# Performance work log

Hardware: AMD Instinct MI355X
Metric: run time of the kernel (lower is better)

## Reference

```python
import math
import jax, jax.numpy as jnp
import numpy as np

SIZE = 512
N_HEADS = 8
HEAD = SIZE // N_HEADS
SCALE = 1.0 / math.sqrt(HEAD)


def setup_inputs() -> dict:
    key = jax.random.key(0)
    ks = jax.random.split(key, 10)
    B, Sq, Skv = 4, 2048, 2048
    std = 1.0 / math.sqrt(SIZE)
    inp = {
        "query": jax.random.normal(ks[0], (B, Sq, SIZE), jnp.float32),
        "key_value": jax.random.normal(ks[1], (B, Skv, SIZE), jnp.float32),
        "Wq": jax.random.normal(ks[2], (SIZE, SIZE), jnp.float32) * std,
        "bq": jax.random.normal(ks[3], (SIZE,), jnp.float32) * std,
        "Wk": jax.random.normal(ks[4], (SIZE, SIZE), jnp.float32) * std,
        "bk": jax.random.normal(ks[5], (SIZE,), jnp.float32) * std,
        "Wv": jax.random.normal(ks[6], (SIZE, SIZE), jnp.float32) * std,
        "bv": jax.random.normal(ks[7], (SIZE,), jnp.float32) * std,
        "Wo": jax.random.normal(ks[8], (SIZE, SIZE), jnp.float32) * std,
        "bo": jax.random.normal(ks[9], (SIZE,), jnp.float32) * std,
    }
    return inp


def reference(query, key_value, Wq, bq, Wk, bk, Wv, bv, Wo, bo):
    B, Sq, D = query.shape
    Skv = key_value.shape[1]
    H, hd = N_HEADS, HEAD

    # Linear projections (torch nn.Linear: x @ W.T + b)
    q = query @ Wq.T + bq            # [B, Sq, D]
    k = key_value @ Wk.T + bk        # [B, Skv, D]
    v = key_value @ Wv.T + bv        # [B, Skv, D]

    # split heads: [B, S, H, hd]
    qh = q.reshape(B, Sq, H, hd)
    kh = k.reshape(B, Skv, H, hd)
    vh = v.reshape(B, Skv, H, hd)

    # attention scores and softmax over keys
    scores = jnp.einsum("bqhd,bkhd->bhqk", qh, kh) * SCALE  # [B, H, Sq, Skv]
    A = jax.nn.softmax(scores, axis=-1)
    o = jnp.einsum("bhqk,bkhd->bqhd", A, vh)                 # [B, Sq, H, hd]

    # residual with q heads (clean_path=False), merge heads
    out = (qh + o).reshape(B, Sq, D)

    # output residual + ReLU FFN stage
    out = out + jax.nn.relu(out @ Wo.T + bo)
    return out
```

## Files before the change

kernel.cpp:

```cpp
#include <hip/hip_runtime.h>
#include <hip/hip_bf16.h>

typedef __hip_bfloat16 bf16;
typedef __attribute__((ext_vector_type(4))) float f32x4;
typedef __attribute__((ext_vector_type(16))) float f32x16;
typedef __attribute__((ext_vector_type(8))) __bf16 bf16x8;

#define DEVI static __device__ __forceinline__

DEVI void gload_lds16(const void* g, void* l) {
  __builtin_amdgcn_global_load_lds(
      (const __attribute__((address_space(1))) void*)g,
      (__attribute__((address_space(3))) void*)l, 16, 0, 0);
}

DEVI unsigned pkbf(float a, float b) {
  union { __hip_bfloat162 h2; unsigned u; } t;
  t.h2.x = __float2bfloat16(a);
  t.h2.y = __float2bfloat16(b);
  return t.u;
}

union PK4 { bf16 h[4]; unsigned long long ll; };

DEVI unsigned long long pack4(float4 v) {
  PK4 u;
  u.h[0] = __float2bfloat16(v.x); u.h[1] = __float2bfloat16(v.y);
  u.h[2] = __float2bfloat16(v.z); u.h[3] = __float2bfloat16(v.w);
  return u.ll;
}

__global__ void cvt2_kernel(const float* __restrict__ a, const float* __restrict__ b,
                            bf16* __restrict__ oa, bf16* __restrict__ ob, int n4) {
  int i = blockIdx.x * blockDim.x + threadIdx.x;
  if (i >= n4) return;
  float4 va = reinterpret_cast<const float4*>(a)[i];
  float4 vb = reinterpret_cast<const float4*>(b)[i];
  reinterpret_cast<unsigned long long*>(oa)[i] = pack4(va);
  reinterpret_cast<unsigned long long*>(ob)[i] = pack4(vb);
}

__global__ void cvt4_kernel(const float* __restrict__ a, const float* __restrict__ b,
                            const float* __restrict__ c, const float* __restrict__ d,
                            bf16* __restrict__ oa, bf16* __restrict__ ob,
                            bf16* __restrict__ oc, bf16* __restrict__ od, int n4) {
  int i = blockIdx.x * blockDim.x + threadIdx.x;
  if (i >= n4) return;
  reinterpret_cast<unsigned long long*>(oa)[i] = pack4(reinterpret_cast<const float4*>(a)[i]);
  reinterpret_cast<unsigned long long*>(ob)[i] = pack4(reinterpret_cast<const float4*>(b)[i]);
  reinterpret_cast<unsigned long long*>(oc)[i] = pack4(reinterpret_cast<const float4*>(c)[i]);
  reinterpret_cast<unsigned long long*>(od)[i] = pack4(reinterpret_cast<const float4*>(d)[i]);
}

__global__ __launch_bounds__(256) void gemm_qkv(
    const bf16* __restrict__ qb, const bf16* __restrict__ kvb,
    const bf16* __restrict__ wqb, const bf16* __restrict__ wkb, const bf16* __restrict__ wvb,
    const float* __restrict__ bq, const float* __restrict__ bk, const float* __restrict__ bv,
    bf16* __restrict__ qp, bf16* __restrict__ kp, bf16* __restrict__ vT) {
  constexpr int K = 512;
  __shared__ __align__(16) char smem[32768];
  char* As = smem;
  char* Bs = smem + 16384;
  const int tid = threadIdx.x;
  const int wave = tid >> 6, lane = tid & 63;
  const int bm = blockIdx.x;
  const int zone = blockIdx.y >> 2, bn = blockIdx.y & 3;
  const bf16* A = zone ? kvb : qb;
  const bf16* W = (zone == 0) ? wqb : (zone == 1 ? wkb : wvb);
  const float* bias = (zone == 0) ? bq : (zone == 1 ? bk : bv);
  const int wm = (wave >> 1) * 64, wn = (wave & 1) * 64;
  const int srow8 = lane >> 3, sslot = lane & 7;

  f32x4 acc[4][4] = {};
  const long Abase = (long)bm * 128 * K;
  const long Wbase = (long)bn * 128 * K;

  for (int kt = 0; kt < K; kt += 64) {
#pragma unroll
    for (int i = 0; i < 4; ++i) {
      int c = wave * 4 + i;
      int row = c * 8 + srow8;
      int gs = sslot ^ (row & 7);
      gload_lds16(A + Abase + (long)row * K + kt + gs * 8, As + c * 1024);
      gload_lds16(W + Wbase + (long)row * K + kt + gs * 8, Bs + c * 1024);
    }
    __syncthreads();
#pragma unroll
    for (int ks = 0; ks < 2; ++ks) {
      bf16x8 af[4], bfv[4];
      int slot = ks * 4 + (lane >> 4);
#pragma unroll
      for (int f = 0; f < 4; ++f) {
        int rowA = wm + f * 16 + (lane & 15);
        af[f] = *reinterpret_cast<const bf16x8*>(As + rowA * 128 + ((slot ^ (rowA & 7)) << 4));
        int rowB = wn + f * 16 + (lane & 15);
        bfv[f] = *reinterpret_cast<const bf16x8*>(Bs + rowB * 128 + ((slot ^ (rowB & 7)) << 4));
      }
#pragma unroll
      for (int mf = 0; mf < 4; ++mf)
#pragma unroll
        for (int nf = 0; nf < 4; ++nf)
          acc[mf][nf] = __builtin_amdgcn_mfma_f32_16x16x32_bf16(af[mf], bfv[nf], acc[mf][nf], 0, 0, 0);
    }
    __syncthreads();
  }

#pragma unroll
  for (int nf = 0; nf < 4; ++nf) {
    int col = bn * 128 + wn + nf * 16 + (lane & 15);
    float bia = bias[col];
#pragma unroll
    for (int mf = 0; mf < 4; ++mf) {
#pragma unroll
      for (int j = 0; j < 4; ++j) {
        int row = bm * 128 + wm + mf * 16 + (lane >> 4) * 4 + j;
        float v = acc[mf][nf][j] + bia;
        if (zone < 2) {
          bf16* Ob = zone ? kp : qp;
          Ob[(long)row * 512 + col] = __float2bfloat16(v);
        } else {
          int b = row >> 11, s = row & 2047;
          int h = col >> 6, d = col & 63;
          vT[((long)((b * 8 + h) * 64 + d)) * 2048 + s] = __float2bfloat16(v);
        }
      }
    }
  }
}

__global__ __launch_bounds__(256) void gemm_ffn(
    const bf16* __restrict__ A, const bf16* __restrict__ W,
    const float* __restrict__ bias, float* __restrict__ Of) {
  constexpr int K = 512;
  __shared__ __align__(16) char smem[24576];
  char* As = smem;
  char* Bs = smem + 8192;
  const int tid = threadIdx.x;
  const int wave = tid >> 6, lane = tid & 63;
  const int bm = blockIdx.x, bn = blockIdx.y;
  const int wm = (wave >> 1) * 32, wn = (wave & 1) * 64;
  const int srow8 = lane >> 3, sslot = lane & 7;

  f32x4 acc[2][4] = {};
  const long Abase = (long)bm * 64 * K;
  const long Wbase = (long)bn * 128 * K;

  for (int kt = 0; kt < K; kt += 64) {
#pragma unroll
    for (int i = 0; i < 2; ++i) {
      int c = wave * 2 + i;
      int row = c * 8 + srow8;
      int gs = sslot ^ (row & 7);
      gload_lds16(A + Abase + (long)row * K + kt + gs * 8, As + c * 1024);
    }
#pragma unroll
    for (int i = 0; i < 4; ++i) {
      int c = wave * 4 + i;
      int row = c * 8 + srow8;
      int gs = sslot ^ (row & 7);
      gload_lds16(W + Wbase + (long)row * K + kt + gs * 8, Bs + c * 1024);
    }
    __syncthreads();
#pragma unroll
    for (int ks = 0; ks < 2; ++ks) {
      bf16x8 af[2], bfv[4];
      int slot = ks * 4 + (lane >> 4);
#pragma unroll
      for (int f = 0; f < 2; ++f) {
        int rowA = wm + f * 16 + (lane & 15);
        af[f] = *reinterpret_cast<const bf16x8*>(As + rowA * 128 + ((slot ^ (rowA & 7)) << 4));
      }
#pragma unroll
      for (int f = 0; f < 4; ++f) {
        int rowB = wn + f * 16 + (lane & 15);
        bfv[f] = *reinterpret_cast<const bf16x8*>(Bs + rowB * 128 + ((slot ^ (rowB & 7)) << 4));
      }
#pragma unroll
      for (int mf = 0; mf < 2; ++mf)
#pragma unroll
        for (int nf = 0; nf < 4; ++nf)
          acc[mf][nf] = __builtin_amdgcn_mfma_f32_16x16x32_bf16(af[mf], bfv[nf], acc[mf][nf], 0, 0, 0);
    }
    __syncthreads();
  }

#pragma unroll
  for (int nf = 0; nf < 4; ++nf) {
    int col = bn * 128 + wn + nf * 16 + (lane & 15);
    float bia = bias[col];
#pragma unroll
    for (int mf = 0; mf < 2; ++mf) {
#pragma unroll
      for (int j = 0; j < 4; ++j) {
        int row = bm * 64 + wm + mf * 16 + (lane >> 4) * 4 + j;
        float r = __bfloat162float(A[(long)row * 512 + col]);
        Of[(long)row * 512 + col] = r + fmaxf(acc[mf][nf][j] + bia, 0.f);
      }
    }
  }
}

__global__ __launch_bounds__(256) void attn_k(
    const bf16* __restrict__ Q, const bf16* __restrict__ Kp,
    const bf16* __restrict__ VT, bf16* __restrict__ O) {
  __shared__ __align__(16) char smem[32768];
  const int tid = threadIdx.x, wave = tid >> 6, lane = tid & 63;
  const int bh = blockIdx.y, b = bh >> 3, h = bh & 7;
  const int q0 = blockIdx.x * 128 + wave * 32;
  const int ql = lane & 31, hl = lane >> 5;
  const long qg = ((long)(b * 2048 + q0 + ql)) * 512 + h * 64;
  const int srow8 = lane >> 3, sslot = lane & 7;

  bf16x8 qf[4];
#pragma unroll
  for (int c = 0; c < 4; ++c)
    qf[c] = *reinterpret_cast<const bf16x8*>(Q + qg + c * 16 + hl * 8);

  f32x16 oacc[2] = {};
  float m = -INFINITY, l = 0.f;
  const float CEXP = 0.125f * 1.44269504088896f;

#define STAGE(BUF, T)                                                                   \
  {                                                                                     \
    char* Ksb = smem + (BUF) * 16384;                                                   \
    char* Vsb = Ksb + 8192;                                                             \
    _Pragma("unroll") for (int i = 0; i < 2; ++i) {                                     \
      int c = wave * 2 + i;                                                             \
      int row = c * 8 + srow8;                                                          \
      int gs = sslot ^ (row & 7);                                                       \
      gload_lds16(Kp + ((long)(b * 2048 + (T) * 64 + row)) * 512 + h * 64 + gs * 8,     \
                  Ksb + c * 1024);                                                      \
      gload_lds16(VT + ((long)(bh * 64 + row)) * 2048 + (T) * 64 + gs * 8,              \
                  Vsb + c * 1024);                                                      \
    }                                                                                   \
  }

  STAGE(0, 0)

  for (int t = 0; t < 32; ++t) {
    const int cur = t & 1;
    if (t < 31) {
      STAGE(cur ^ 1, t + 1)
      asm volatile("s_waitcnt vmcnt(4)" ::: "memory");
    } else {
      asm volatile("s_waitcnt vmcnt(0)" ::: "memory");
    }
    asm volatile("s_barrier" ::: "memory");

    char* Ksb = smem + cur * 16384;
    char* Vsb = Ksb + 8192;

    f32x16 sacc[2] = {};
    __builtin_amdgcn_s_setprio(1);
#pragma unroll
    for (int s = 0; s < 2; ++s) {
#pragma unroll
      for (int c = 0; c < 4; ++c) {
        int row = s * 32 + ql;
        bf16x8 kf = *reinterpret_cast<const bf16x8*>(
            Ksb + row * 128 + (((c * 2 + hl) ^ (row & 7)) << 4));
        sacc[s] = __builtin_amdgcn_mfma_f32_32x32x16_bf16(kf, qf[c], sacc[s], 0, 0, 0);
      }
    }
    __builtin_amdgcn_s_setprio(0);

    float pmax = -3.0e38f;
#pragma unroll
    for (int s = 0; s < 2; ++s)
#pragma unroll
      for (int i = 0; i < 16; ++i) pmax = fmaxf(pmax, sacc[s][i]);
    pmax = fmaxf(pmax, __shfl_xor(pmax, 32));

    if (!__all(pmax - m <= 44.3614195558365f)) {
      float mn = fmaxf(m, pmax);
      float al = exp2f((m - mn) * CEXP);
      m = mn;
      l *= al;
#pragma unroll
      for (int d = 0; d < 2; ++d)
#pragma unroll
        for (int i = 0; i < 16; ++i) oacc[d][i] *= al;
    }
    float nmC = -m * CEXP;
    float p[32];
    float ps = 0.f;
#pragma unroll
    for (int s = 0; s < 2; ++s)
#pragma unroll
      for (int i = 0; i < 16; ++i) {
        float pv = exp2f(fmaf(sacc[s][i], CEXP, nmC));
        p[s * 16 + i] = pv;
        ps += pv;
      }
    ps += __shfl_xor(ps, 32);
    l += ps;

    __builtin_amdgcn_s_setprio(1);
#pragma unroll
    for (int s = 0; s < 2; ++s) {
#pragma unroll
      for (int jj = 0; jj < 2; ++jj) {
        int base = s * 16 + jj * 8;
        unsigned w0 = pkbf(p[base + 0], p[base + 1]);
        unsigned w1 = pkbf(p[base + 2], p[base + 3]);
        unsigned w2 = pkbf(p[base + 4], p[base + 5]);
        unsigned w3 = pkbf(p[base + 6], p[base + 7]);
        asm("v_permlane32_swap_b32 %0, %1" : "+v"(w0), "+v"(w2));
        asm("v_permlane32_swap_b32 %0, %1" : "+v"(w1), "+v"(w3));
        union { unsigned u[4]; bf16x8 v; } pf;
        pf.u[0] = w0; pf.u[1] = w1; pf.u[2] = w2; pf.u[3] = w3;
        int j = s * 2 + jj;
#pragma unroll
        for (int dblk = 0; dblk < 2; ++dblk) {
          int row = dblk * 32 + ql;
          bf16x8 vf = *reinterpret_cast<const bf16x8*>(
              Vsb + row * 128 + (((j * 2 + hl) ^ (row & 7)) << 4));
          oacc[dblk] = __builtin_amdgcn_mfma_f32_32x32x16_bf16(vf, pf.v, oacc[dblk], 0, 0, 0);
        }
      }
    }
    __builtin_amdgcn_s_setprio(0);

    asm volatile("s_barrier" ::: "memory");
  }

  float rl = 1.0f / l;
#pragma unroll
  for (int dblk = 0; dblk < 2; ++dblk) {
#pragma unroll
    for (int g = 0; g < 4; ++g) {
      int d0 = dblk * 32 + g * 8 + hl * 4;
      const long ga = qg + d0;
      union { ushort4 s; unsigned short u[4]; } qin, ov;
      qin.s = *reinterpret_cast<const ushort4*>(Q + ga);
#pragma unroll
      for (int i = 0; i < 4; ++i) {
        float qvf = __uint_as_float((unsigned)qin.u[i] << 16);
        float r = qvf + oacc[dblk][g * 4 + i] * rl;
        bf16 hb = __float2bfloat16(r);
        ov.u[i] = *reinterpret_cast<unsigned short*>(&hb);
      }
      *reinterpret_cast<ushort4*>(O + ga) = ov.s;
    }
  }
}

extern "C" void kernel_launch(void* const* d_in, const int* in_sizes, int n_in,
                              void* d_out, int out_size, void* d_ws, size_t ws_size,
                              hipStream_t stream) {
  const float* query = (const float*)d_in[0];
  const float* keyv  = (const float*)d_in[1];
  const float* Wq = (const float*)d_in[2];
  const float* bq = (const float*)d_in[3];
  const float* Wk = (const float*)d_in[4];
  const float* bk = (const float*)d_in[5];
  const float* Wv = (const float*)d_in[6];
  const float* bv = (const float*)d_in[7];
  const float* Wo = (const float*)d_in[8];
  const float* bo = (const float*)d_in[9];
  float* out = (float*)d_out;
  char* ws = (char*)d_ws;

  bf16* qb  = (bf16*)(ws + 0);
  bf16* kvb = (bf16*)(ws + 8388608);
  bf16* wqb = (bf16*)(ws + 16777216);
  bf16* wkb = (bf16*)(ws + 17301504);
  bf16* wvb = (bf16*)(ws + 17825792);
  bf16* wob = (bf16*)(ws + 18350080);
  bf16* qp  = (bf16*)(ws + 18874368);
  bf16* kp  = (bf16*)(ws + 27262976);
  bf16* vT  = (bf16*)(ws + 35651584);
  bf16* o1  = (bf16*)(ws + 44040192);

  cvt2_kernel<<<4096, 256, 0, stream>>>(query, keyv, qb, kvb, 1048576);
  cvt4_kernel<<<256, 256, 0, stream>>>(Wq, Wk, Wv, Wo, wqb, wkb, wvb, wob, 65536);

  gemm_qkv<<<dim3(64, 12), 256, 0, stream>>>(qb, kvb, wqb, wkb, wvb, bq, bk, bv, qp, kp, vT);

  attn_k<<<dim3(16, 32), 256, 0, stream>>>(qp, kp, vT, o1);

  gemm_ffn<<<dim3(128, 4), 256, 0, stream>>>(o1, wob, bo, out);
}
```

Measured before the change: 220.6 us.

## Double-buffer GEMM loads, merge convert kernels, vectorize V^T stores, MFMA row-sum

Both projection GEMMs now double-buffer their shared-memory tiles, issuing the next K-slice's global-to-LDS loads before computing on the current one. The loop uses precomputed pointers and offsets, explicit vmcnt waits and raw barriers. The two fp32-to-bf16 conversion kernels are merged into one launch, and the V-transpose epilogue writes four bf16 values per store instead of scalar stores. In attention, the softmax row sum is accumulated with an MFMA against a ones vector instead of a scalar reduction with a shuffle, and the key loop is unrolled by two with precomputed offsets. The GEMMs now use twice the LDS per block, which may reduce occupancy, and the ones-MFMA sums bf16-rounded probabilities.

```diff
diff --git a/kernel.cpp b/kernel.cpp
--- a/kernel.cpp
+++ b/kernel.cpp
@@ -30,26 +30,24 @@
   return u.ll;
 }
 
-__global__ void cvt2_kernel(const float* __restrict__ a, const float* __restrict__ b,
-                            bf16* __restrict__ oa, bf16* __restrict__ ob, int n4) {
-  int i = blockIdx.x * blockDim.x + threadIdx.x;
-  if (i >= n4) return;
-  float4 va = reinterpret_cast<const float4*>(a)[i];
-  float4 vb = reinterpret_cast<const float4*>(b)[i];
-  reinterpret_cast<unsigned long long*>(oa)[i] = pack4(va);
-  reinterpret_cast<unsigned long long*>(ob)[i] = pack4(vb);
-}
-
-__global__ void cvt4_kernel(const float* __restrict__ a, const float* __restrict__ b,
-                            const float* __restrict__ c, const float* __restrict__ d,
-                            bf16* __restrict__ oa, bf16* __restrict__ ob,
-                            bf16* __restrict__ oc, bf16* __restrict__ od, int n4) {
-  int i = blockIdx.x * blockDim.x + threadIdx.x;
-  if (i >= n4) return;
-  reinterpret_cast<unsigned long long*>(oa)[i] = pack4(reinterpret_cast<const float4*>(a)[i]);
-  reinterpret_cast<unsigned long long*>(ob)[i] = pack4(reinterpret_cast<const float4*>(b)[i]);
-  reinterpret_cast<unsigned long long*>(oc)[i] = pack4(reinterpret_cast<const float4*>(c)[i]);
-  reinterpret_cast<unsigned long long*>(od)[i] = pack4(reinterpret_cast<const float4*>(d)[i]);
+__global__ void cvt_all(const float* __restrict__ q, const float* __restrict__ kv,
+                        const float* __restrict__ wq, const float* __restrict__ wk,
+                        const float* __restrict__ wv, const float* __restrict__ wo,
+                        bf16* __restrict__ oq, bf16* __restrict__ okv,
+                        bf16* __restrict__ owq, bf16* __restrict__ owk,
+                        bf16* __restrict__ owv, bf16* __restrict__ owo) {
+  int bid = blockIdx.x;
+  if (bid < 4096) {
+    int i = bid * 256 + threadIdx.x;
+    reinterpret_cast<unsigned long long*>(oq)[i]  = pack4(reinterpret_cast<const float4*>(q)[i]);
+    reinterpret_cast<unsigned long long*>(okv)[i] = pack4(reinterpret_cast<const float4*>(kv)[i]);
+  } else {
+    int i = (bid - 4096) * 256 + threadIdx.x;
+    reinterpret_cast<unsigned long long*>(owq)[i] = pack4(reinterpret_cast<const float4*>(wq)[i]);
+    reinterpret_cast<unsigned long long*>(owk)[i] = pack4(reinterpret_cast<const float4*>(wk)[i]);
+    reinterpret_cast<unsigned long long*>(owv)[i] = pack4(reinterpret_cast<const float4*>(wv)[i]);
+    reinterpret_cast<unsigned long long*>(owo)[i] = pack4(reinterpret_cast<const float4*>(wo)[i]);
+  }
 }
 
 __global__ __launch_bounds__(256) void gemm_qkv(
@@ -58,9 +56,7 @@
     const float* __restrict__ bq, const float* __restrict__ bk, const float* __restrict__ bv,
     bf16* __restrict__ qp, bf16* __restrict__ kp, bf16* __restrict__ vT) {
   constexpr int K = 512;
-  __shared__ __align__(16) char smem[32768];
-  char* As = smem;
-  char* Bs = smem + 16384;
+  __shared__ __align__(16) char smem[65536];
   const int tid = threadIdx.x;
   const int wave = tid >> 6, lane = tid & 63;
   const int bm = blockIdx.x;
@@ -72,38 +68,73 @@
   const int srow8 = lane >> 3, sslot = lane & 7;
 
   f32x4 acc[4][4] = {};
-  const long Abase = (long)bm * 128 * K;
-  const long Wbase = (long)bn * 128 * K;
-
-  for (int kt = 0; kt < K; kt += 64) {
-#pragma unroll
-    for (int i = 0; i < 4; ++i) {
-      int c = wave * 4 + i;
-      int row = c * 8 + srow8;
-      int gs = sslot ^ (row & 7);
-      gload_lds16(A + Abase + (long)row * K + kt + gs * 8, As + c * 1024);
-      gload_lds16(W + Wbase + (long)row * K + kt + gs * 8, Bs + c * 1024);
-    }
-    __syncthreads();
-#pragma unroll
-    for (int ks = 0; ks < 2; ++ks) {
-      bf16x8 af[4], bfv[4];
-      int slot = ks * 4 + (lane >> 4);
-#pragma unroll
-      for (int f = 0; f < 4; ++f) {
-        int rowA = wm + f * 16 + (lane & 15);
-        af[f] = *reinterpret_cast<const bf16x8*>(As + rowA * 128 + ((slot ^ (rowA & 7)) << 4));
-        int rowB = wn + f * 16 + (lane & 15);
-        bfv[f] = *reinterpret_cast<const bf16x8*>(Bs + rowB * 128 + ((slot ^ (rowB & 7)) << 4));
-      }
-#pragma unroll
-      for (int mf = 0; mf < 4; ++mf)
-#pragma unroll
-        for (int nf = 0; nf < 4; ++nf)
-          acc[mf][nf] = __builtin_amdgcn_mfma_f32_16x16x32_bf16(af[mf], bfv[nf], acc[mf][nf], 0, 0, 0);
-    }
-    __syncthreads();
-  }
+
+  const bf16* ap[4];
+  const bf16* wp[4];
+  char* adst[4];
+  char* bdst[4];
+#pragma unroll
+  for (int i = 0; i < 4; ++i) {
+    int c = wave * 4 + i;
+    int row = c * 8 + srow8;
+    int gs = sslot ^ (row & 7);
+    ap[i] = A + (long)(bm * 128 + row) * K + gs * 8;
+    wp[i] = W + (long)(bn * 128 + row) * K + gs * 8;
+    adst[i] = smem + c * 1024;
+    bdst[i] = smem + 16384 + c * 1024;
+  }
+
+  int aoff[2][4], boff[2][4];
+#pragma unroll
+  for (int ks = 0; ks < 2; ++ks)
+#pragma unroll
+    for (int f = 0; f < 4; ++f) {
+      int r = f * 16 + (lane & 15);
+      int sw = ((ks * 4 + (lane >> 4)) ^ (r & 7)) << 4;
+      aoff[ks][f] = (wm + r) * 128 + sw;
+      boff[ks][f] = (wn + r) * 128 + sw;
+    }
+
+#define GSTAGE(BUF)                                                       \
+  _Pragma("unroll") for (int i = 0; i < 4; ++i) {                         \
+    gload_lds16(ap[i], adst[i] + (BUF) * 32768);                          \
+    gload_lds16(wp[i], bdst[i] + (BUF) * 32768);                          \
+    ap[i] += 64; wp[i] += 64;                                             \
+  }
+
+#define GBODY(BUF, LAST)                                                  \
+  {                                                                       \
+    if (!(LAST)) {                                                        \
+      GSTAGE((BUF) ^ 1)                                                   \
+      asm volatile("s_waitcnt vmcnt(8)" ::: "memory");                    \
+    } else {                                                              \
+      asm volatile("s_waitcnt vmcnt(0)" ::: "memory");                    \
+    }                                                                     \
+    asm volatile("s_barrier" ::: "memory");                               \
+    const char* Asb = smem + (BUF) * 32768;                               \
+    const char* Bsb = Asb + 16384;                                        \
+    _Pragma("unroll") for (int ks = 0; ks < 2; ++ks) {                    \
+      bf16x8 af[4], bfv[4];                                               \
+      _Pragma("unroll") for (int f = 0; f < 4; ++f) {                     \
+        af[f]  = *reinterpret_cast<const bf16x8*>(Asb + aoff[ks][f]);     \
+        bfv[f] = *reinterpret_cast<const bf16x8*>(Bsb + boff[ks][f]);     \
+      }                                                                   \
+      _Pragma("unroll") for (int mf = 0; mf < 4; ++mf)                    \
+        _Pragma("unroll") for (int nf = 0; nf < 4; ++nf)                  \
+          acc[mf][nf] = __builtin_amdgcn_mfma_f32_16x16x32_bf16(          \
+              af[mf], bfv[nf], acc[mf][nf], 0, 0, 0);                     \
+    }                                                                     \
+    asm volatile("s_barrier" ::: "memory");                               \
+  }
+
+  GSTAGE(0)
+#pragma unroll 1
+  for (int kt = 0; kt < 8; kt += 2) {
+    GBODY(0, false)
+    GBODY(1, kt + 1 == 7)
+  }
+#undef GSTAGE
+#undef GBODY
 
 #pragma unroll
   for (int nf = 0; nf < 4; ++nf) {
@@ -111,18 +142,22 @@
     float bia = bias[col];
 #pragma unroll
     for (int mf = 0; mf < 4; ++mf) {
-#pragma unroll
-      for (int j = 0; j < 4; ++j) {
-        int row = bm * 128 + wm + mf * 16 + (lane >> 4) * 4 + j;
-        float v = acc[mf][nf][j] + bia;
-        if (zone < 2) {
-          bf16* Ob = zone ? kp : qp;
-          Ob[(long)row * 512 + col] = __float2bfloat16(v);
-        } else {
-          int b = row >> 11, s = row & 2047;
-          int h = col >> 6, d = col & 63;
-          vT[((long)((b * 8 + h) * 64 + d)) * 2048 + s] = __float2bfloat16(v);
+      int row0 = bm * 128 + wm + mf * 16 + (lane >> 4) * 4;
+      if (zone < 2) {
+        bf16* Ob = zone ? kp : qp;
+#pragma unroll
+        for (int j = 0; j < 4; ++j)
+          Ob[(long)(row0 + j) * 512 + col] = __float2bfloat16(acc[mf][nf][j] + bia);
+      } else {
+        int b = row0 >> 11, s0 = row0 & 2047;
+        int h = col >> 6, d = col & 63;
+        union { ushort4 s; unsigned short u[4]; } pk;
+#pragma unroll
+        for (int j = 0; j < 4; ++j) {
+          bf16 hv = __float2bfloat16(acc[mf][nf][j] + bia);
+          pk.u[j] = *reinterpret_cast<unsigned short*>(&hv);
         }
+        *reinterpret_cast<ushort4*>(vT + ((long)((b * 8 + h) * 64 + d)) * 2048 + s0) = pk.s;
       }
     }
   }
@@ -132,9 +167,7 @@
     const bf16* __restrict__ A, const bf16* __restrict__ W,
     const float* __restrict__ bias, float* __restrict__ Of) {
   constexpr int K = 512;
-  __shared__ __align__(16) char smem[24576];
-  char* As = smem;
-  char* Bs = smem + 8192;
+  __shared__ __align__(16) char smem[49152];
   const int tid = threadIdx.x;
   const int wave = tid >> 6, lane = tid & 63;
   const int bm = blockIdx.x, bn = blockIdx.y;
@@ -142,47 +175,88 @@
   const int srow8 = lane >> 3, sslot = lane & 7;
 
   f32x4 acc[2][4] = {};
-  const long Abase = (long)bm * 64 * K;
-  const long Wbase = (long)bn * 128 * K;
-
-  for (int kt = 0; kt < K; kt += 64) {
-#pragma unroll
-    for (int i = 0; i < 2; ++i) {
-      int c = wave * 2 + i;
-      int row = c * 8 + srow8;
-      int gs = sslot ^ (row & 7);
-      gload_lds16(A + Abase + (long)row * K + kt + gs * 8, As + c * 1024);
-    }
-#pragma unroll
-    for (int i = 0; i < 4; ++i) {
-      int c = wave * 4 + i;
-      int row = c * 8 + srow8;
-      int gs = sslot ^ (row & 7);
-      gload_lds16(W + Wbase + (long)row * K + kt + gs * 8, Bs + c * 1024);
-    }
-    __syncthreads();
-#pragma unroll
-    for (int ks = 0; ks < 2; ++ks) {
-      bf16x8 af[2], bfv[4];
-      int slot = ks * 4 + (lane >> 4);
-#pragma unroll
-      for (int f = 0; f < 2; ++f) {
-        int rowA = wm + f * 16 + (lane & 15);
-        af[f] = *reinterpret_cast<const bf16x8*>(As + rowA * 128 + ((slot ^ (rowA & 7)) << 4));
-      }
-#pragma unroll
-      for (int f = 0; f < 4; ++f) {
-        int rowB = wn + f * 16 + (lane & 15);
-        bfv[f] = *reinterpret_cast<const bf16x8*>(Bs + rowB * 128 + ((slot ^ (rowB & 7)) << 4));
-      }
-#pragma unroll
-      for (int mf = 0; mf < 2; ++mf)
-#pragma unroll
-        for (int nf = 0; nf < 4; ++nf)
-          acc[mf][nf] = __builtin_amdgcn_mfma_f32_16x16x32_bf16(af[mf], bfv[nf], acc[mf][nf], 0, 0, 0);
-    }
-    __syncthreads();
-  }
+
+  const bf16* ap[2];
+  const bf16* wp[4];
+  char* adst[2];
+  char* bdst[4];
+#pragma unroll
+  for (int i = 0; i < 2; ++i) {
+    int c = wave * 2 + i;
+    int row = c * 8 + srow8;
+    int gs = sslot ^ (row & 7);
+    ap[i] = A + (long)(bm * 64 + row) * K + gs * 8;
+    adst[i] = smem + c * 1024;
+  }
+#pragma unroll
+  for (int i = 0; i < 4; ++i) {
+    int c = wave * 4 + i;
+    int row = c * 8 + srow8;
+    int gs = sslot ^ (row & 7);
+    wp[i] = W + (long)(bn * 128 + row) * K + gs * 8;
+    bdst[i] = smem + 8192 + c * 1024;
+  }
+
+  int aoff[2][2], boff[2][4];
+#pragma unroll
+  for (int ks = 0; ks < 2; ++ks) {
+#pragma unroll
+    for (int f = 0; f < 2; ++f) {
+      int r = f * 16 + (lane & 15);
+      aoff[ks][f] = (wm + r) * 128 + (((ks * 4 + (lane >> 4)) ^ (r & 7)) << 4);
+    }
+#pragma unroll
+    for (int f = 0; f < 4; ++f) {
+      int r = f * 16 + (lane & 15);
+      boff[ks][f] = (wn + r) * 128 + (((ks * 4 + (lane >> 4)) ^ (r & 7)) << 4);
+    }
+  }
+
+#define FSTAGE(BUF)                                                       \
+  {                                                                       \
+    _Pragma("unroll") for (int i = 0; i < 2; ++i) {                       \
+      gload_lds16(ap[i], adst[i] + (BUF) * 24576);                        \
+      ap[i] += 64;                                                        \
+    }                                                                     \
+    _Pragma("unroll") for (int i = 0; i < 4; ++i) {                       \
+      gload_lds16(wp[i], bdst[i] + (BUF) * 24576);                        \
+      wp[i] += 64;                                                        \
+    }                                                                     \
+  }
+
+#define FBODY(BUF, LAST)                                                  \
+  {                                                                       \
+    if (!(LAST)) {                                                        \
+      FSTAGE((BUF) ^ 1)                                                   \
+      asm volatile("s_waitcnt vmcnt(6)" ::: "memory");                    \
+    } else {                                                              \
+      asm volatile("s_waitcnt vmcnt(0)" ::: "memory");                    \
+    }                                                                     \
+    asm volatile("s_barrier" ::: "memory");                               \
+    const char* Asb = smem + (BUF) * 24576;                               \
+    const char* Bsb = Asb + 8192;                                         \
+    _Pragma("unroll") for (int ks = 0; ks < 2; ++ks) {                    \
+      bf16x8 af[2], bfv[4];                                               \
+      _Pragma("unroll") for (int f = 0; f < 2; ++f)                       \
+        af[f] = *reinterpret_cast<const bf16x8*>(Asb + aoff[ks][f]);      \
+      _Pragma("unroll") for (int f = 0; f < 4; ++f)                       \
+        bfv[f] = *reinterpret_cast<const bf16x8*>(Bsb + boff[ks][f]);     \
+      _Pragma("unroll") for (int mf = 0; mf < 2; ++mf)                    \
+        _Pragma("unroll") for (int nf = 0; nf < 4; ++nf)                  \
+          acc[mf][nf] = __builtin_amdgcn_mfma_f32_16x16x32_bf16(          \
+              af[mf], bfv[nf], acc[mf][nf], 0, 0, 0);                     \
+    }                                                                     \
+    asm volatile("s_barrier" ::: "memory");                               \
+  }
+
+  FSTAGE(0)
+#pragma unroll 1
+  for (int kt = 0; kt < 8; kt += 2) {
+    FBODY(0, false)
+    FBODY(1, kt + 1 == 7)
+  }
+#undef FSTAGE
+#undef FBODY
 
 #pragma unroll
   for (int nf = 0; nf < 4; ++nf) {
@@ -216,115 +290,120 @@
   for (int c = 0; c < 4; ++c)
     qf[c] = *reinterpret_cast<const bf16x8*>(Q + qg + c * 16 + hl * 8);
 
+  bf16x8 ones;
+#pragma unroll
+  for (int j = 0; j < 8; ++j) ones[j] = (__bf16)1.0f;
+
   f32x16 oacc[2] = {};
-  float m = -INFINITY, l = 0.f;
+  f32x16 lacc = {};
+  float m = -INFINITY;
   const float CEXP = 0.125f * 1.44269504088896f;
 
-#define STAGE(BUF, T)                                                                   \
-  {                                                                                     \
-    char* Ksb = smem + (BUF) * 16384;                                                   \
-    char* Vsb = Ksb + 8192;                                                             \
-    _Pragma("unroll") for (int i = 0; i < 2; ++i) {                                     \
-      int c = wave * 2 + i;                                                             \
-      int row = c * 8 + srow8;                                                          \
-      int gs = sslot ^ (row & 7);                                                       \
-      gload_lds16(Kp + ((long)(b * 2048 + (T) * 64 + row)) * 512 + h * 64 + gs * 8,     \
-                  Ksb + c * 1024);                                                      \
-      gload_lds16(VT + ((long)(bh * 64 + row)) * 2048 + (T) * 64 + gs * 8,              \
-                  Vsb + c * 1024);                                                      \
-    }                                                                                   \
-  }
-
-  STAGE(0, 0)
-
-  for (int t = 0; t < 32; ++t) {
-    const int cur = t & 1;
-    if (t < 31) {
-      STAGE(cur ^ 1, t + 1)
-      asm volatile("s_waitcnt vmcnt(4)" ::: "memory");
-    } else {
-      asm volatile("s_waitcnt vmcnt(0)" ::: "memory");
-    }
-    asm volatile("s_barrier" ::: "memory");
-
-    char* Ksb = smem + cur * 16384;
-    char* Vsb = Ksb + 8192;
-
-    f32x16 sacc[2] = {};
-    __builtin_amdgcn_s_setprio(1);
-#pragma unroll
-    for (int s = 0; s < 2; ++s) {
-#pragma unroll
-      for (int c = 0; c < 4; ++c) {
-        int row = s * 32 + ql;
-        bf16x8 kf = *reinterpret_cast<const bf16x8*>(
-            Ksb + row * 128 + (((c * 2 + hl) ^ (row & 7)) << 4));
-        sacc[s] = __builtin_amdgcn_mfma_f32_32x32x16_bf16(kf, qf[c], sacc[s], 0, 0, 0);
-      }
-    }
-    __builtin_amdgcn_s_setprio(0);
-
-    float pmax = -3.0e38f;
-#pragma unroll
-    for (int s = 0; s < 2; ++s)
-#pragma unroll
-      for (int i = 0; i < 16; ++i) pmax = fmaxf(pmax, sacc[s][i]);
-    pmax = fmaxf(pmax, __shfl_xor(pmax, 32));
-
-    if (!__all(pmax - m <= 44.3614195558365f)) {
-      float mn = fmaxf(m, pmax);
-      float al = exp2f((m - mn) * CEXP);
-      m = mn;
-      l *= al;
-#pragma unroll
-      for (int d = 0; d < 2; ++d)
-#pragma unroll
-        for (int i = 0; i < 16; ++i) oacc[d][i] *= al;
-    }
-    float nmC = -m * CEXP;
-    float p[32];
-    float ps = 0.f;
-#pragma unroll
-    for (int s = 0; s < 2; ++s)
-#pragma unroll
-      for (int i = 0; i < 16; ++i) {
-        float pv = exp2f(fmaf(sacc[s][i], CEXP, nmC));
-        p[s * 16 + i] = pv;
-        ps += pv;
-      }
-    ps += __shfl_xor(ps, 32);
-    l += ps;
-
-    __builtin_amdgcn_s_setprio(1);
-#pragma unroll
-    for (int s = 0; s < 2; ++s) {
-#pragma unroll
-      for (int jj = 0; jj < 2; ++jj) {
-        int base = s * 16 + jj * 8;
-        unsigned w0 = pkbf(p[base + 0], p[base + 1]);
-        unsigned w1 = pkbf(p[base + 2], p[base + 3]);
-        unsigned w2 = pkbf(p[base + 4], p[base + 5]);
-        unsigned w3 = pkbf(p[base + 6], p[base + 7]);
-        asm("v_permlane32_swap_b32 %0, %1" : "+v"(w0), "+v"(w2));
-        asm("v_permlane32_swap_b32 %0, %1" : "+v"(w1), "+v"(w3));
-        union { unsigned u[4]; bf16x8 v; } pf;
-        pf.u[0] = w0; pf.u[1] = w1; pf.u[2] = w2; pf.u[3] = w3;
-        int j = s * 2 + jj;
-#pragma unroll
-        for (int dblk = 0; dblk < 2; ++dblk) {
-          int row = dblk * 32 + ql;
-          bf16x8 vf = *reinterpret_cast<const bf16x8*>(
-              Vsb + row * 128 + (((j * 2 + hl) ^ (row & 7)) << 4));
-          oacc[dblk] = __builtin_amdgcn_mfma_f32_32x32x16_bf16(vf, pf.v, oacc[dblk], 0, 0, 0);
-        }
-      }
-    }
-    __builtin_amdgcn_s_setprio(0);
-
-    asm volatile("s_barrier" ::: "memory");
-  }
-
-  float rl = 1.0f / l;
+  const bf16* kgp[2];
+  const bf16* vgp[2];
+  char* kdst[2];
+  char* vdst[2];
+#pragma unroll
+  for (int i = 0; i < 2; ++i) {
+    int c = wave * 2 + i;
+    int row = c * 8 + srow8;
+    int gs = sslot ^ (row & 7);
+    kgp[i] = Kp + ((long)(b * 2048 + row)) * 512 + h * 64 + gs * 8;
+    vgp[i] = VT + ((long)(bh * 64 + row)) * 2048 + gs * 8;
+    kdst[i] = smem + c * 1024;
+    vdst[i] = smem + 8192 + c * 1024;
+  }
+
+  int ofs[2][4];
+#pragma unroll
+  for (int s = 0; s < 2; ++s)
+#pragma unroll
+    for (int c = 0; c < 4; ++c) {
+      int row = s * 32 + ql;
+      ofs[s][c] = row * 128 + (((c * 2 + hl) ^ (row & 7)) << 4);
+    }
+
+#define ASTAGE(BUF)                                                       \
+  _Pragma("unroll") for (int i = 0; i < 2; ++i) {                         \
+    gload_lds16(kgp[i], kdst[i] + (BUF) * 16384);                         \
+    gload_lds16(vgp[i], vdst[i] + (BUF) * 16384);                         \
+    kgp[i] += 32768; vgp[i] += 64;                                        \
+  }
+
+#define ABODY(BUF, LAST)                                                  \
+  {                                                                       \
+    if (!(LAST)) {                                                        \
+      ASTAGE((BUF) ^ 1)                                                   \
+      asm volatile("s_waitcnt vmcnt(4)" ::: "memory");                    \
+    } else {                                                              \
+      asm volatile("s_waitcnt vmcnt(0)" ::: "memory");                    \
+    }                                                                     \
+    asm volatile("s_barrier" ::: "memory");                               \
+    const char* Kb = smem + (BUF) * 16384;                                \
+    const char* Vb = Kb + 8192;                                           \
+    f32x16 sacc[2] = {};                                                  \
+    __builtin_amdgcn_s_setprio(1);                                        \
+    _Pragma("unroll") for (int s = 0; s < 2; ++s)                         \
+      _Pragma("unroll") for (int c = 0; c < 4; ++c) {                     \
+        bf16x8 kf = *reinterpret_cast<const bf16x8*>(Kb + ofs[s][c]);     \
+        sacc[s] = __builtin_amdgcn_mfma_f32_32x32x16_bf16(                \
+            kf, qf[c], sacc[s], 0, 0, 0);                                 \
+      }                                                                   \
+    __builtin_amdgcn_s_setprio(0);                                        \
+    float pmax = fmaxf(sacc[0][0], sacc[0][1]);                           \
+    _Pragma("unroll") for (int i = 2; i < 16; i += 2)                     \
+      pmax = fmaxf(fmaxf(pmax, sacc[0][i]), sacc[0][i + 1]);              \
+    _Pragma("unroll") for (int i = 0; i < 16; i += 2)                     \
+      pmax = fmaxf(fmaxf(pmax, sacc[1][i]), sacc[1][i + 1]);              \
+    pmax = fmaxf(pmax, __shfl_xor(pmax, 32));                             \
+    if (!__all(pmax - m <= 44.3614195558365f)) {                          \
+      float mn = fmaxf(m, pmax);                                          \
+      float al = exp2f((m - mn) * CEXP);                                  \
+      m = mn;                                                             \
+      _Pragma("unroll") for (int i = 0; i < 16; ++i) {                    \
+        oacc[0][i] *= al; oacc[1][i] *= al; lacc[i] *= al;                \
+      }                                                                   \
+    }                                                                     \
+    float nmC = -m * CEXP;                                                \
+    float p[32];                                                          \
+    _Pragma("unroll") for (int s = 0; s < 2; ++s)                         \
+      _Pragma("unroll") for (int i = 0; i < 16; ++i)                      \
+        p[s * 16 + i] = exp2f(fmaf(sacc[s][i], CEXP, nmC));               \
+    __builtin_amdgcn_s_setprio(1);                                        \
+    _Pragma("unroll") for (int s = 0; s < 2; ++s)                         \
+      _Pragma("unroll") for (int jj = 0; jj < 2; ++jj) {                  \
+        int base = s * 16 + jj * 8;                                       \
+        unsigned w0 = pkbf(p[base + 0], p[base + 1]);                     \
+        unsigned w1 = pkbf(p[base + 2], p[base + 3]);                     \
+        unsigned w2 = pkbf(p[base + 4], p[base + 5]);                     \
+        unsigned w3 = pkbf(p[base + 6], p[base + 7]);                     \
+        asm("v_permlane32_swap_b32 %0, %1" : "+v"(w0), "+v"(w2));         \
+        asm("v_permlane32_swap_b32 %0, %1" : "+v"(w1), "+v"(w3));         \
+        union { unsigned u[4]; bf16x8 v; } pf;                            \
+        pf.u[0] = w0; pf.u[1] = w1; pf.u[2] = w2; pf.u[3] = w3;           \
+        lacc = __builtin_amdgcn_mfma_f32_32x32x16_bf16(                   \
+            ones, pf.v, lacc, 0, 0, 0);                                   \
+        int j = s * 2 + jj;                                               \
+        _Pragma("unroll") for (int dblk = 0; dblk < 2; ++dblk) {          \
+          bf16x8 vf = *reinterpret_cast<const bf16x8*>(Vb + ofs[dblk][j]);\
+          oacc[dblk] = __builtin_amdgcn_mfma_f32_32x32x16_bf16(           \
+              vf, pf.v, oacc[dblk], 0, 0, 0);                             \
+        }                                                                 \
+      }                                                                   \
+    __builtin_amdgcn_s_setprio(0);                                        \
+    asm volatile("s_barrier" ::: "memory");                               \
+  }
+
+  ASTAGE(0)
+#pragma unroll 1
+  for (int tt = 0; tt < 16; ++tt) {
+    ABODY(0, false)
+    ABODY(1, tt == 15)
+  }
+#undef ASTAGE
+#undef ABODY
+
+  float rl = 1.0f / lacc[0];
 #pragma unroll
   for (int dblk = 0; dblk < 2; ++dblk) {
 #pragma unroll
@@ -372,8 +451,8 @@
   bf16* vT  = (bf16*)(ws + 35651584);
   bf16* o1  = (bf16*)(ws + 44040192);
 
-  cvt2_kernel<<<4096, 256, 0, stream>>>(query, keyv, qb, kvb, 1048576);
-  cvt4_kernel<<<256, 256, 0, stream>>>(Wq, Wk, Wv, Wo, wqb, wkb, wvb, wob, 65536);
+  cvt_all<<<4352, 256, 0, stream>>>(query, keyv, Wq, Wk, Wv, Wo,
+                                    qb, kvb, wqb, wkb, wvb, wob);
 
   gemm_qkv<<<dim3(64, 12), 256, 0, stream>>>(qb, kvb, wqb, wkb, wvb, bq, bk, bv, qp, kp, vT);
 
```

Measured after the change: 193.0 us. -12.5%, faster.
